# Kernel tuning notes

Hardware: AMD Instinct MI355X
Metric: run time of the kernel (lower is better)

Reference implementation:

```python
import jax, jax.numpy as jnp
import numpy as np

B, N, DIM = 8, 1024, 1024
H, DH = 16, 64           # heads, dim_head; inner_dim = H*DH = 1024
SCALE = DH ** -0.5


def setup_inputs() -> dict:
    key = jax.random.key(0)
    k_x, k_qkv, k_out, k_b = jax.random.split(key, 4)
    inner = H * DH
    x = jax.random.normal(k_x, (B, N, DIM), dtype=jnp.float32)
    # nn.Linear(dim, inner*3, bias=False): y = x @ W_qkv
    W_qkv = jax.random.normal(k_qkv, (DIM, 3 * inner), dtype=jnp.float32) * (DIM ** -0.5)
    # nn.Linear(inner, dim) with bias (project_out is True since heads!=1)
    W_out = jax.random.normal(k_out, (inner, DIM), dtype=jnp.float32) * (inner ** -0.5)
    b_out = jax.random.normal(k_b, (DIM,), dtype=jnp.float32) * 0.01
    return {"x": x, "W_qkv": W_qkv, "W_out": W_out, "b_out": b_out}


def reference(x, W_qkv, W_out, b_out):
    # 'trans' branch of Attention.forward (dropout p=0 -> identity)
    qkv = x @ W_qkv                                   # [b, n, 3*inner]
    q, k, v = jnp.split(qkv, 3, axis=-1)              # each [b, n, inner]
    def to_heads(t):
        b, n, _ = t.shape
        return t.reshape(b, n, H, DH).transpose(0, 2, 1, 3)  # [b, h, n, d]
    q, k, v = to_heads(q), to_heads(k), to_heads(v)
    dots = jnp.einsum('bhid,bhjd->bhij', q, k) * SCALE  # [b, h, n, n]
    attn = jax.nn.softmax(dots, axis=-1)
    out = jnp.einsum('bhij,bhjd->bhid', attn, v)        # [b, h, n, d]
    # original sets attn = out (b h n d) before merging heads
    attn_ret = out
    out_m = out.transpose(0, 2, 1, 3).reshape(B, N, H * DH)  # [b, n, inner]
    proj = out_m @ W_out + b_out                        # [b, n, dim]
    return (proj, attn_ret)
```

## Files before the change

kernel.cpp:

```cpp
#include <hip/hip_runtime.h>
#include <hip/hip_bf16.h>
#include <math.h>

typedef __bf16 bf16_t;
typedef __bf16 bf16x8 __attribute__((ext_vector_type(8)));
typedef __bf16 bf16x4 __attribute__((ext_vector_type(4)));
typedef float f32x4 __attribute__((ext_vector_type(4)));

#define MFMA16(a, b, c) __builtin_amdgcn_mfma_f32_16x16x32_bf16((a), (b), (c), 0, 0, 0)

#define AS3(p) ((__attribute__((address_space(3))) void*)(p))
#define AS1(p) ((const __attribute__((address_space(1))) void*)(p))

#define B_ 8
#define N_ 1024
#define DIM_ 1024
#define H_ 16
#define DH_ 64

#define QSCALE 0.18033688011112042f
#define SM_SHIFT 12.0f

__global__ __launch_bounds__(256) void k_prep(const float* __restrict__ x,
                                              bf16_t* __restrict__ xb,
                                              const float* __restrict__ Wqkv,
                                              bf16_t* __restrict__ wqkvt,
                                              const float* __restrict__ Wout,
                                              bf16_t* __restrict__ woutt) {
    int bx = blockIdx.x;
    int tid = threadIdx.x;
    if (bx < 4096) {
        size_t idx = ((size_t)bx * 256 + tid) * 8;
        f32x4 a = *(const f32x4*)(x + idx);
        f32x4 b = *(const f32x4*)(x + idx + 4);
        bf16x8 o;
        o[0] = (bf16_t)a[0]; o[1] = (bf16_t)a[1]; o[2] = (bf16_t)a[2]; o[3] = (bf16_t)a[3];
        o[4] = (bf16_t)b[0]; o[5] = (bf16_t)b[1]; o[6] = (bf16_t)b[2]; o[7] = (bf16_t)b[3];
        *(bf16x8*)(xb + idx) = o;
        return;
    }
    __shared__ float tile[32][33];
    int idx = bx - 4096;
    int rb = idx >> 7, cbx = idx & 127;
    const float* in;
    bf16_t* out;
    int C, cb;
    if (cbx < 96) { in = Wqkv; out = wqkvt; C = 3072; cb = cbx; }
    else          { in = Wout; out = woutt; C = 1024; cb = cbx - 96; }
    const int R = 1024;
    int c0 = cb * 32, r0 = rb * 32;
    int tx = tid & 31, ty = tid >> 5;
#pragma unroll
    for (int i = 0; i < 4; ++i)
        tile[ty + 8 * i][tx] = in[(size_t)(r0 + ty + 8 * i) * C + (c0 + tx)];
    __syncthreads();
#pragma unroll
    for (int i = 0; i < 4; ++i)
        out[(size_t)(c0 + ty + 8 * i) * R + (r0 + tx)] = (bf16_t)tile[tx][ty + 8 * i];
}

__global__ __launch_bounds__(512, 1) void k_gemm_qkv(const bf16_t* __restrict__ A,
                                                     const bf16_t* __restrict__ Bt,
                                                     bf16_t* __restrict__ qb,
                                                     bf16_t* __restrict__ kbuf,
                                                     bf16_t* __restrict__ vbuf) {
    __shared__ __align__(16) bf16_t As[2][256 * 64];
    __shared__ __align__(16) bf16_t Bs[2][256 * 64];
    int tid = threadIdx.x;
    int lane = tid & 63, wave = tid >> 6;
    int quad = lane >> 4, l16 = lane & 15;
    int wr = wave >> 2, wc = wave & 3;

    int bid = blockIdx.x;
    int swz = (bid & 7) * 48 + (bid >> 3);
    int mt = swz / 12, nt = swz % 12;
    int m0 = mt * 256, c0 = nt * 256;

    const f32x4 vzero = {0.f, 0.f, 0.f, 0.f};
    f32x4 acc[8][4];
#pragma unroll
    for (int i = 0; i < 8; ++i)
#pragma unroll
        for (int j = 0; j < 4; ++j) acc[i][j] = vzero;

    int s0 = ((quad) ^ (l16 & 7)) * 8;
    int s1 = ((4 + quad) ^ (l16 & 7)) * 8;

    auto stageA = [&](int t, int i) {
        int k0 = t * 64;
        bf16_t* Ad = &As[t & 1][0];
        int cid = tid + 512 * i;
        int row = cid >> 3;
        int g = (cid & 7) ^ (row & 7);
        __builtin_amdgcn_global_load_lds(
            AS1(A + (size_t)(m0 + row) * 1024 + k0 + g * 8), AS3(Ad + cid * 8), 16, 0, 0);
    };
    auto stageB = [&](int t, int i) {
        int k0 = t * 64;
        bf16_t* Bd = &Bs[t & 1][0];
        int cid = tid + 512 * i;
        int row = cid >> 3;
        int g = (cid & 7) ^ (row & 7);
        __builtin_amdgcn_global_load_lds(
            AS1(Bt + (size_t)(c0 + row) * 1024 + k0 + g * 8), AS3(Bd + cid * 8), 16, 0, 0);
    };
    auto stage_all = [&](int t) {
#pragma unroll
        for (int i = 0; i < 4; ++i) stageA(t, i);
#pragma unroll
        for (int i = 0; i < 4; ++i) stageB(t, i);
    };

    stage_all(0);
    stage_all(1);

#pragma unroll 2
    for (int t = 0; t < 16; ++t) {
        int cur = t & 1;
        if (t < 15)
            asm volatile("s_waitcnt vmcnt(8)" ::: "memory");
        else
            asm volatile("s_waitcnt vmcnt(0)" ::: "memory");
        __builtin_amdgcn_s_barrier();
        asm volatile("" ::: "memory");

        const bf16_t* Arow = &As[cur][0] + (size_t)(wr * 128 + l16) * 64;
        const bf16_t* Brow = &Bs[cur][0] + (size_t)(wc * 64 + l16) * 64;
        bool pre = (t + 2 < 16);

        bf16x8 af[4][2], bq0[2][2], bq1[2][2];

#pragma unroll
        for (int i = 0; i < 4; ++i) {
            af[i][0] = *(const bf16x8*)(Arow + (16 * i) * 64 + s0);
            af[i][1] = *(const bf16x8*)(Arow + (16 * i) * 64 + s1);
        }
#pragma unroll
        for (int j = 0; j < 2; ++j) {
            bq0[j][0] = *(const bf16x8*)(Brow + (16 * j) * 64 + s0);
            bq0[j][1] = *(const bf16x8*)(Brow + (16 * j) * 64 + s1);
        }
        asm volatile("" ::: "memory");
        __builtin_amdgcn_s_barrier();
        asm volatile("s_waitcnt lgkmcnt(0)" ::: "memory");
        __builtin_amdgcn_sched_barrier(0);
        __builtin_amdgcn_s_setprio(1);
#pragma unroll
        for (int i = 0; i < 4; ++i)
#pragma unroll
            for (int j = 0; j < 2; ++j) {
                acc[i][j] = MFMA16(af[i][0], bq0[j][0], acc[i][j]);
                acc[i][j] = MFMA16(af[i][1], bq0[j][1], acc[i][j]);
            }
        __builtin_amdgcn_s_setprio(0);
        asm volatile("" ::: "memory");
        __builtin_amdgcn_s_barrier();

#pragma unroll
        for (int j = 0; j < 2; ++j) {
            bq1[j][0] = *(const bf16x8*)(Brow + (32 + 16 * j) * 64 + s0);
            bq1[j][1] = *(const bf16x8*)(Brow + (32 + 16 * j) * 64 + s1);
        }
        if (pre) { stageA(t + 2, 0); stageA(t + 2, 2); }
        asm volatile("" ::: "memory");
        __builtin_amdgcn_s_barrier();
        asm volatile("s_waitcnt lgkmcnt(0)" ::: "memory");
        __builtin_amdgcn_sched_barrier(0);
        __builtin_amdgcn_s_setprio(1);
#pragma unroll
        for (int i = 0; i < 4; ++i)
#pragma unroll
            for (int j = 0; j < 2; ++j) {
                acc[i][2 + j] = MFMA16(af[i][0], bq1[j][0], acc[i][2 + j]);
                acc[i][2 + j] = MFMA16(af[i][1], bq1[j][1], acc[i][2 + j]);
            }
        __builtin_amdgcn_s_setprio(0);
        asm volatile("" ::: "memory");
        __builtin_amdgcn_s_barrier();

#pragma unroll
        for (int i = 0; i < 4; ++i) {
            af[i][0] = *(const bf16x8*)(Arow + (64 + 16 * i) * 64 + s0);
            af[i][1] = *(const bf16x8*)(Arow + (64 + 16 * i) * 64 + s1);
        }
        if (pre) {
#pragma unroll
            for (int i = 0; i < 4; ++i) stageB(t + 2, i);
        }
        asm volatile("" ::: "memory");
        __builtin_amdgcn_s_barrier();
        asm volatile("s_waitcnt lgkmcnt(0)" ::: "memory");
        __builtin_amdgcn_sched_barrier(0);
        __builtin_amdgcn_s_setprio(1);
#pragma unroll
        for (int i = 0; i < 4; ++i)
#pragma unroll
            for (int j = 0; j < 2; ++j) {
                acc[4 + i][2 + j] = MFMA16(af[i][0], bq1[j][0], acc[4 + i][2 + j]);
                acc[4 + i][2 + j] = MFMA16(af[i][1], bq1[j][1], acc[4 + i][2 + j]);
            }
        __builtin_amdgcn_s_setprio(0);
        asm volatile("" ::: "memory");
        __builtin_amdgcn_s_barrier();

        if (pre) { stageA(t + 2, 1); stageA(t + 2, 3); }
        asm volatile("" ::: "memory");
        __builtin_amdgcn_s_barrier();
        __builtin_amdgcn_sched_barrier(0);
        __builtin_amdgcn_s_setprio(1);
#pragma unroll
        for (int i = 0; i < 4; ++i)
#pragma unroll
            for (int j = 0; j < 2; ++j) {
                acc[4 + i][j] = MFMA16(af[i][0], bq0[j][0], acc[4 + i][j]);
                acc[4 + i][j] = MFMA16(af[i][1], bq0[j][1], acc[4 + i][j]);
            }
        __builtin_amdgcn_s_setprio(0);
        asm volatile("" ::: "memory");
        __builtin_amdgcn_s_barrier();
    }

    int tsel = nt >> 2;
    bf16_t* obase = (tsel == 0) ? qb : (tsel == 1) ? kbuf : vbuf;
    float scl = (tsel == 0) ? QSCALE : 1.0f;
#pragma unroll
    for (int i = 0; i < 8; ++i) {
#pragma unroll
        for (int r = 0; r < 4; ++r) {
            int m = m0 + wr * 128 + 16 * i + quad * 4 + r;
            int b = m >> 10, n = m & 1023;
#pragma unroll
            for (int j = 0; j < 4; ++j) {
                int cc = c0 + wc * 64 + 16 * j + l16;
                int ic = cc & 1023;
                int h = ic >> 6, d = ic & 63;
                obase[(((size_t)b * H_ + h) * N_ + n) * DH_ + d] = (bf16_t)(acc[i][j][r] * scl);
            }
        }
    }
}

__global__ __launch_bounds__(256) void k_prep_v(const bf16_t* __restrict__ in,
                                                bf16_t* __restrict__ out) {
    __shared__ bf16_t t[64][65];
    int bh = blockIdx.y;
    int n0 = blockIdx.x * 64;
    int tid = threadIdx.x;
    int r = tid >> 2, c = (tid & 3) * 16;
    const bf16_t* ip = in + ((size_t)bh * N_ + n0 + r) * DH_ + c;
    bf16x8 a = *(const bf16x8*)ip;
    bf16x8 b2 = *(const bf16x8*)(ip + 8);
#pragma unroll
    for (int e = 0; e < 8; ++e) { t[r][c + e] = a[e]; t[r][c + 8 + e] = b2[e]; }
    __syncthreads();
    bf16x8 o1, o2;
#pragma unroll
    for (int e = 0; e < 8; ++e) { o1[e] = t[c + e][r]; o2[e] = t[c + 8 + e][r]; }
    bf16_t* op = out + ((size_t)bh * DH_ + r) * N_ + n0 + c;
    *(bf16x8*)op = o1;
    *(bf16x8*)(op + 8) = o2;
}

__global__ __launch_bounds__(256, 2) void k_attn(const bf16_t* __restrict__ q,
                                                 const bf16_t* __restrict__ k,
                                                 const bf16_t* __restrict__ vt,
                                                 float* __restrict__ oattn,
                                                 bf16_t* __restrict__ outm) {
    __shared__ __align__(16) bf16_t Ks[64 * 64];
    __shared__ __align__(16) bf16_t Vs[64 * 64];
    __shared__ __align__(16) bf16_t Ps[4 * 4 * 16 * 72];
    int tid = threadIdx.x;
    int lane = tid & 63, wave = tid >> 6;
    int quad = lane >> 4, l16 = lane & 15;
    int qt = blockIdx.x & 3;
    int bh = blockIdx.x >> 2;
    int b = bh >> 4, h = bh & 15;

    const bf16_t* qp = q + ((size_t)bh * N_ + qt * 256 + wave * 64) * DH_;
    bf16x8 qa[4][2];
#pragma unroll
    for (int g = 0; g < 4; ++g)
#pragma unroll
        for (int c = 0; c < 2; ++c)
            qa[g][c] = *(const bf16x8*)(qp + (size_t)(g * 16 + l16) * DH_ + c * 32 + quad * 8);

    const bf16_t* kp = k + (size_t)bh * N_ * DH_;
    const bf16_t* vp = vt + (size_t)bh * DH_ * N_;
    bf16_t* Pw = Ps + wave * (4 * 16 * 72);

    const f32x4 vzero = {0.f, 0.f, 0.f, 0.f};
    f32x4 o[4][4];
#pragma unroll
    for (int g = 0; g < 4; ++g)
#pragma unroll
        for (int t = 0; t < 4; ++t) o[g][t] = vzero;
    float lsum[4] = {0.f, 0.f, 0.f, 0.f};

    for (int kb = 0; kb < 16; ++kb) {
#pragma unroll
        for (int i = 0; i < 2; ++i) {
            int cid = tid + 256 * i;
            int row = cid >> 3;
            int g = (cid & 7) ^ (row & 7);
            __builtin_amdgcn_global_load_lds(
                AS1(kp + (size_t)(kb * 64 + row) * DH_ + g * 8), AS3(Ks + cid * 8), 16, 0, 0);
            __builtin_amdgcn_global_load_lds(
                AS1(vp + (size_t)row * N_ + kb * 64 + g * 8), AS3(Vs + cid * 8), 16, 0, 0);
        }
        __syncthreads();

        f32x4 st[4][4];
#pragma unroll
        for (int jt = 0; jt < 4; ++jt) {
#pragma unroll
            for (int g = 0; g < 4; ++g) st[g][jt] = vzero;
#pragma unroll
            for (int c = 0; c < 2; ++c) {
                int s = (4 * c + quad) ^ (l16 & 7);
                bf16x8 kf = *(const bf16x8*)(Ks + (16 * jt + l16) * 64 + s * 8);
#pragma unroll
                for (int g = 0; g < 4; ++g)
                    st[g][jt] = MFMA16(kf, qa[g][c], st[g][jt]);
            }
        }

#pragma unroll
        for (int g = 0; g < 4; ++g) {
            float ps = 0.f;
#pragma unroll
            for (int jt = 0; jt < 4; ++jt) {
                bf16x4 pk;
#pragma unroll
                for (int r = 0; r < 4; ++r) {
                    float p = __builtin_amdgcn_exp2f(st[g][jt][r] - SM_SHIFT);
                    ps += p;
                    pk[r] = (bf16_t)p;
                }
                *(bf16x4*)(Pw + g * (16 * 72) + l16 * 72 + jt * 16 + quad * 4) = pk;
            }
            lsum[g] += ps;
        }

        bf16x8 pf[4][2];
#pragma unroll
        for (int g = 0; g < 4; ++g)
#pragma unroll
            for (int c = 0; c < 2; ++c)
                pf[g][c] = *(const bf16x8*)(Pw + g * (16 * 72) + l16 * 72 + c * 32 + quad * 8);
#pragma unroll
        for (int t = 0; t < 4; ++t)
#pragma unroll
            for (int c = 0; c < 2; ++c) {
                int s = (4 * c + quad) ^ (l16 & 7);
                bf16x8 vf = *(const bf16x8*)(Vs + (16 * t + l16) * 64 + s * 8);
#pragma unroll
                for (int g = 0; g < 4; ++g)
                    o[g][t] = MFMA16(vf, pf[g][c], o[g][t]);
            }
        __syncthreads();
    }

#pragma unroll
    for (int g = 0; g < 4; ++g) {
        lsum[g] += __shfl_xor(lsum[g], 16);
        lsum[g] += __shfl_xor(lsum[g], 32);
    }

    float* Ot = (float*)Ps + wave * 16 * 68;
#pragma unroll
    for (int g = 0; g < 4; ++g) {
        float inv = 1.f / lsum[g];
#pragma unroll
        for (int t = 0; t < 4; ++t) {
            f32x4 v4;
#pragma unroll
            for (int r = 0; r < 4; ++r) v4[r] = o[g][t][r] * inv;
            *(f32x4*)(Ot + l16 * 68 + t * 16 + quad * 4) = v4;
        }
        int row = lane >> 2, cl = lane & 3;
        int n = qt * 256 + wave * 64 + g * 16 + row;
        const float* orow = Ot + row * 68 + cl * 16;
        float* gout = oattn + ((size_t)bh * N_ + n) * DH_ + cl * 16;
        bf16_t* gm = outm + ((size_t)b * N_ + n) * DIM_ + h * DH_ + cl * 16;
#pragma unroll
        for (int s = 0; s < 4; ++s) {
            f32x4 v = *(const f32x4*)(orow + s * 4);
            *(f32x4*)(gout + s * 4) = v;
            bf16x4 vb;
#pragma unroll
            for (int r = 0; r < 4; ++r) vb[r] = (bf16_t)v[r];
            *(bf16x4*)(gm + s * 4) = vb;
        }
    }
}

__global__ __launch_bounds__(256) void k_gemm_proj(const bf16_t* __restrict__ A,
                                                   const bf16_t* __restrict__ Bt,
                                                   const float* __restrict__ bias,
                                                   float* __restrict__ out) {
    __shared__ __align__(16) bf16_t As[128 * 64];
    __shared__ __align__(16) bf16_t Bs[128 * 64];
    int tid = threadIdx.x;
    int lane = tid & 63, wave = tid >> 6;
    int quad = lane >> 4, l16 = lane & 15;
    int m0 = blockIdx.y * 128, c0 = blockIdx.x * 128;
    int wm = (wave & 1) * 64, wn = (wave >> 1) * 64;

    const f32x4 vzero = {0.f, 0.f, 0.f, 0.f};
    f32x4 acc[4][4];
#pragma unroll
    for (int i = 0; i < 4; ++i)
#pragma unroll
        for (int j = 0; j < 4; ++j) acc[i][j] = vzero;

    for (int k0 = 0; k0 < 1024; k0 += 64) {
#pragma unroll
        for (int i = 0; i < 4; ++i) {
            int cid = tid + 256 * i;
            int row = cid >> 3;
            int g = (cid & 7) ^ (row & 7);
            __builtin_amdgcn_global_load_lds(
                AS1(A + (size_t)(m0 + row) * 1024 + k0 + g * 8), AS3(As + cid * 8), 16, 0, 0);
            __builtin_amdgcn_global_load_lds(
                AS1(Bt + (size_t)(c0 + row) * 1024 + k0 + g * 8), AS3(Bs + cid * 8), 16, 0, 0);
        }
        __syncthreads();
#pragma unroll
        for (int c = 0; c < 2; ++c) {
            int s = (4 * c + quad) ^ (l16 & 7);
            bf16x8 bfr[4];
#pragma unroll
            for (int j = 0; j < 4; ++j)
                bfr[j] = *(const bf16x8*)(Bs + (wn + 16 * j + l16) * 64 + s * 8);
#pragma unroll
            for (int i = 0; i < 4; ++i) {
                bf16x8 af = *(const bf16x8*)(As + (wm + 16 * i + l16) * 64 + s * 8);
#pragma unroll
                for (int j = 0; j < 4; ++j)
                    acc[i][j] = MFMA16(af, bfr[j], acc[i][j]);
            }
        }
        __syncthreads();
    }

#pragma unroll
    for (int i = 0; i < 4; ++i) {
#pragma unroll
        for (int r = 0; r < 4; ++r) {
            int m = m0 + wm + 16 * i + quad * 4 + r;
#pragma unroll
            for (int j = 0; j < 4; ++j) {
                int cc = c0 + wn + 16 * j + l16;
                out[(size_t)m * DIM_ + cc] = acc[i][j][r] + bias[cc];
            }
        }
    }
}

extern "C" void kernel_launch(void* const* d_in, const int* in_sizes, int n_in,
                              void* d_out, int out_size, void* d_ws, size_t ws_size,
                              hipStream_t stream) {
    const float* x    = (const float*)d_in[0];
    const float* Wqkv = (const float*)d_in[1];
    const float* Wout = (const float*)d_in[2];
    const float* bout = (const float*)d_in[3];

    float* proj  = (float*)d_out;
    float* oattn = proj + (size_t)B_ * N_ * DIM_;

    char* ws = (char*)d_ws;
    const size_t MB = 1024 * 1024;
    bf16_t* xb    = (bf16_t*)(ws);
    bf16_t* wqkvt = (bf16_t*)(ws + 16 * MB);
    bf16_t* woutt = (bf16_t*)(ws + 22 * MB);
    bf16_t* qb    = (bf16_t*)(ws + 24 * MB);
    bf16_t* kbuf  = (bf16_t*)(ws + 40 * MB);
    bf16_t* vtb   = (bf16_t*)(ws + 56 * MB);
    bf16_t* outm  = (bf16_t*)(ws + 72 * MB);
    bf16_t* vbuf  = outm;

    k_prep<<<8192, 256, 0, stream>>>(x, xb, Wqkv, wqkvt, Wout, woutt);
    k_gemm_qkv<<<384, 512, 0, stream>>>(xb, wqkvt, qb, kbuf, vbuf);
    k_prep_v<<<dim3(16, 128), 256, 0, stream>>>(vbuf, vtb);
    k_attn<<<512, 256, 0, stream>>>(qb, kbuf, vtb, oattn, outm);
    k_gemm_proj<<<dim3(8, 64), 256, 0, stream>>>(outm, woutt, bout, proj);
}
```

Measured before the change: 253.5 us.

## Retile QKV GEMM to 256x192, double-buffer attention KV and projection GEMM

```diff
diff --git a/kernel.cpp b/kernel.cpp
--- a/kernel.cpp
+++ b/kernel.cpp
@@ -65,23 +65,23 @@
                                                      bf16_t* __restrict__ kbuf,
                                                      bf16_t* __restrict__ vbuf) {
     __shared__ __align__(16) bf16_t As[2][256 * 64];
-    __shared__ __align__(16) bf16_t Bs[2][256 * 64];
+    __shared__ __align__(16) bf16_t Bs[2][192 * 64];
     int tid = threadIdx.x;
     int lane = tid & 63, wave = tid >> 6;
     int quad = lane >> 4, l16 = lane & 15;
     int wr = wave >> 2, wc = wave & 3;
 
     int bid = blockIdx.x;
-    int swz = (bid & 7) * 48 + (bid >> 3);
-    int mt = swz / 12, nt = swz % 12;
-    int m0 = mt * 256, c0 = nt * 256;
+    int swz = (bid & 7) * 64 + (bid >> 3);
+    int mt = swz >> 4, nt = swz & 15;
+    int m0 = mt * 256, c0 = nt * 192;
 
     const f32x4 vzero = {0.f, 0.f, 0.f, 0.f};
-    f32x4 acc[8][4];
+    f32x4 acc[8][3];
 #pragma unroll
     for (int i = 0; i < 8; ++i)
 #pragma unroll
-        for (int j = 0; j < 4; ++j) acc[i][j] = vzero;
+        for (int j = 0; j < 3; ++j) acc[i][j] = vzero;
 
     int s0 = ((quad) ^ (l16 & 7)) * 8;
     int s1 = ((4 + quad) ^ (l16 & 7)) * 8;
@@ -108,7 +108,7 @@
 #pragma unroll
         for (int i = 0; i < 4; ++i) stageA(t, i);
 #pragma unroll
-        for (int i = 0; i < 4; ++i) stageB(t, i);
+        for (int i = 0; i < 3; ++i) stageB(t, i);
     };
 
     stage_all(0);
@@ -118,17 +118,17 @@
     for (int t = 0; t < 16; ++t) {
         int cur = t & 1;
         if (t < 15)
-            asm volatile("s_waitcnt vmcnt(8)" ::: "memory");
+            asm volatile("s_waitcnt vmcnt(7)" ::: "memory");
         else
             asm volatile("s_waitcnt vmcnt(0)" ::: "memory");
         __builtin_amdgcn_s_barrier();
         asm volatile("" ::: "memory");
 
         const bf16_t* Arow = &As[cur][0] + (size_t)(wr * 128 + l16) * 64;
-        const bf16_t* Brow = &Bs[cur][0] + (size_t)(wc * 64 + l16) * 64;
+        const bf16_t* Brow = &Bs[cur][0] + (size_t)(wc * 48 + l16) * 64;
         bool pre = (t + 2 < 16);
 
-        bf16x8 af[4][2], bq0[2][2], bq1[2][2];
+        bf16x8 af[4][2], bq[2][2], b2[2];
 
 #pragma unroll
         for (int i = 0; i < 4; ++i) {
@@ -137,8 +137,8 @@
         }
 #pragma unroll
         for (int j = 0; j < 2; ++j) {
-            bq0[j][0] = *(const bf16x8*)(Brow + (16 * j) * 64 + s0);
-            bq0[j][1] = *(const bf16x8*)(Brow + (16 * j) * 64 + s1);
+            bq[j][0] = *(const bf16x8*)(Brow + (16 * j) * 64 + s0);
+            bq[j][1] = *(const bf16x8*)(Brow + (16 * j) * 64 + s1);
         }
         asm volatile("" ::: "memory");
         __builtin_amdgcn_s_barrier();
@@ -149,18 +149,15 @@
         for (int i = 0; i < 4; ++i)
 #pragma unroll
             for (int j = 0; j < 2; ++j) {
-                acc[i][j] = MFMA16(af[i][0], bq0[j][0], acc[i][j]);
-                acc[i][j] = MFMA16(af[i][1], bq0[j][1], acc[i][j]);
+                acc[i][j] = MFMA16(af[i][0], bq[j][0], acc[i][j]);
+                acc[i][j] = MFMA16(af[i][1], bq[j][1], acc[i][j]);
             }
         __builtin_amdgcn_s_setprio(0);
         asm volatile("" ::: "memory");
         __builtin_amdgcn_s_barrier();
 
-#pragma unroll
-        for (int j = 0; j < 2; ++j) {
-            bq1[j][0] = *(const bf16x8*)(Brow + (32 + 16 * j) * 64 + s0);
-            bq1[j][1] = *(const bf16x8*)(Brow + (32 + 16 * j) * 64 + s1);
-        }
+        b2[0] = *(const bf16x8*)(Brow + 32 * 64 + s0);
+        b2[1] = *(const bf16x8*)(Brow + 32 * 64 + s1);
         if (pre) { stageA(t + 2, 0); stageA(t + 2, 2); }
         asm volatile("" ::: "memory");
         __builtin_amdgcn_s_barrier();
@@ -168,12 +165,10 @@
         __builtin_amdgcn_sched_barrier(0);
         __builtin_amdgcn_s_setprio(1);
 #pragma unroll
-        for (int i = 0; i < 4; ++i)
-#pragma unroll
-            for (int j = 0; j < 2; ++j) {
-                acc[i][2 + j] = MFMA16(af[i][0], bq1[j][0], acc[i][2 + j]);
-                acc[i][2 + j] = MFMA16(af[i][1], bq1[j][1], acc[i][2 + j]);
-            }
+        for (int i = 0; i < 4; ++i) {
+            acc[i][2] = MFMA16(af[i][0], b2[0], acc[i][2]);
+            acc[i][2] = MFMA16(af[i][1], b2[1], acc[i][2]);
+        }
         __builtin_amdgcn_s_setprio(0);
         asm volatile("" ::: "memory");
         __builtin_amdgcn_s_barrier();
@@ -185,7 +180,7 @@
         }
         if (pre) {
 #pragma unroll
-            for (int i = 0; i < 4; ++i) stageB(t + 2, i);
+            for (int i = 0; i < 3; ++i) stageB(t + 2, i);
         }
         asm volatile("" ::: "memory");
         __builtin_amdgcn_s_barrier();
@@ -193,12 +188,10 @@
         __builtin_amdgcn_sched_barrier(0);
         __builtin_amdgcn_s_setprio(1);
 #pragma unroll
-        for (int i = 0; i < 4; ++i)
-#pragma unroll
-            for (int j = 0; j < 2; ++j) {
-                acc[4 + i][2 + j] = MFMA16(af[i][0], bq1[j][0], acc[4 + i][2 + j]);
-                acc[4 + i][2 + j] = MFMA16(af[i][1], bq1[j][1], acc[4 + i][2 + j]);
-            }
+        for (int i = 0; i < 4; ++i) {
+            acc[4 + i][2] = MFMA16(af[i][0], b2[0], acc[4 + i][2]);
+            acc[4 + i][2] = MFMA16(af[i][1], b2[1], acc[4 + i][2]);
+        }
         __builtin_amdgcn_s_setprio(0);
         asm volatile("" ::: "memory");
         __builtin_amdgcn_s_barrier();
@@ -212,17 +205,14 @@
         for (int i = 0; i < 4; ++i)
 #pragma unroll
             for (int j = 0; j < 2; ++j) {
-                acc[4 + i][j] = MFMA16(af[i][0], bq0[j][0], acc[4 + i][j]);
-                acc[4 + i][j] = MFMA16(af[i][1], bq0[j][1], acc[4 + i][j]);
+                acc[4 + i][j] = MFMA16(af[i][0], bq[j][0], acc[4 + i][j]);
+                acc[4 + i][j] = MFMA16(af[i][1], bq[j][1], acc[4 + i][j]);
             }
         __builtin_amdgcn_s_setprio(0);
         asm volatile("" ::: "memory");
         __builtin_amdgcn_s_barrier();
     }
 
-    int tsel = nt >> 2;
-    bf16_t* obase = (tsel == 0) ? qb : (tsel == 1) ? kbuf : vbuf;
-    float scl = (tsel == 0) ? QSCALE : 1.0f;
 #pragma unroll
     for (int i = 0; i < 8; ++i) {
 #pragma unroll
@@ -230,10 +220,13 @@
             int m = m0 + wr * 128 + 16 * i + quad * 4 + r;
             int b = m >> 10, n = m & 1023;
 #pragma unroll
-            for (int j = 0; j < 4; ++j) {
-                int cc = c0 + wc * 64 + 16 * j + l16;
+            for (int j = 0; j < 3; ++j) {
+                int cc = c0 + wc * 48 + 16 * j + l16;
+                int tsel = cc >> 10;
                 int ic = cc & 1023;
                 int h = ic >> 6, d = ic & 63;
+                bf16_t* obase = (tsel == 0) ? qb : (tsel == 1) ? kbuf : vbuf;
+                float scl = (tsel == 0) ? QSCALE : 1.0f;
                 obase[(((size_t)b * H_ + h) * N_ + n) * DH_ + d] = (bf16_t)(acc[i][j][r] * scl);
             }
         }
@@ -266,8 +259,8 @@
                                                  const bf16_t* __restrict__ vt,
                                                  float* __restrict__ oattn,
                                                  bf16_t* __restrict__ outm) {
-    __shared__ __align__(16) bf16_t Ks[64 * 64];
-    __shared__ __align__(16) bf16_t Vs[64 * 64];
+    __shared__ __align__(16) bf16_t Ks[2][64 * 64];
+    __shared__ __align__(16) bf16_t Vs[2][64 * 64];
     __shared__ __align__(16) bf16_t Ps[4 * 4 * 16 * 72];
     int tid = threadIdx.x;
     int lane = tid & 63, wave = tid >> 6;
@@ -288,26 +281,43 @@
     const bf16_t* vp = vt + (size_t)bh * DH_ * N_;
     bf16_t* Pw = Ps + wave * (4 * 16 * 72);
 
-    const f32x4 vzero = {0.f, 0.f, 0.f, 0.f};
-    f32x4 o[4][4];
-#pragma unroll
-    for (int g = 0; g < 4; ++g)
-#pragma unroll
-        for (int t = 0; t < 4; ++t) o[g][t] = vzero;
-    float lsum[4] = {0.f, 0.f, 0.f, 0.f};
-
-    for (int kb = 0; kb < 16; ++kb) {
+    auto stageKV = [&](int kb) {
 #pragma unroll
         for (int i = 0; i < 2; ++i) {
             int cid = tid + 256 * i;
             int row = cid >> 3;
             int g = (cid & 7) ^ (row & 7);
             __builtin_amdgcn_global_load_lds(
-                AS1(kp + (size_t)(kb * 64 + row) * DH_ + g * 8), AS3(Ks + cid * 8), 16, 0, 0);
+                AS1(kp + (size_t)(kb * 64 + row) * DH_ + g * 8),
+                AS3(&Ks[kb & 1][0] + cid * 8), 16, 0, 0);
             __builtin_amdgcn_global_load_lds(
-                AS1(vp + (size_t)row * N_ + kb * 64 + g * 8), AS3(Vs + cid * 8), 16, 0, 0);
-        }
-        __syncthreads();
+                AS1(vp + (size_t)row * N_ + kb * 64 + g * 8),
+                AS3(&Vs[kb & 1][0] + cid * 8), 16, 0, 0);
+        }
+    };
+
+    const f32x4 vzero = {0.f, 0.f, 0.f, 0.f};
+    f32x4 o[4][4];
+#pragma unroll
+    for (int g = 0; g < 4; ++g)
+#pragma unroll
+        for (int t = 0; t < 4; ++t) o[g][t] = vzero;
+    float lsum[4] = {0.f, 0.f, 0.f, 0.f};
+
+    stageKV(0);
+    stageKV(1);
+
+    for (int kb = 0; kb < 16; ++kb) {
+        int cur = kb & 1;
+        if (kb < 15)
+            asm volatile("s_waitcnt vmcnt(4)" ::: "memory");
+        else
+            asm volatile("s_waitcnt vmcnt(0)" ::: "memory");
+        __builtin_amdgcn_s_barrier();
+        asm volatile("" ::: "memory");
+
+        const bf16_t* Kc = &Ks[cur][0];
+        const bf16_t* Vc = &Vs[cur][0];
 
         f32x4 st[4][4];
 #pragma unroll
@@ -317,7 +327,7 @@
 #pragma unroll
             for (int c = 0; c < 2; ++c) {
                 int s = (4 * c + quad) ^ (l16 & 7);
-                bf16x8 kf = *(const bf16x8*)(Ks + (16 * jt + l16) * 64 + s * 8);
+                bf16x8 kf = *(const bf16x8*)(Kc + (16 * jt + l16) * 64 + s * 8);
 #pragma unroll
                 for (int g = 0; g < 4; ++g)
                     st[g][jt] = MFMA16(kf, qa[g][c], st[g][jt]);
@@ -352,12 +362,16 @@
 #pragma unroll
             for (int c = 0; c < 2; ++c) {
                 int s = (4 * c + quad) ^ (l16 & 7);
-                bf16x8 vf = *(const bf16x8*)(Vs + (16 * t + l16) * 64 + s * 8);
+                bf16x8 vf = *(const bf16x8*)(Vc + (16 * t + l16) * 64 + s * 8);
 #pragma unroll
                 for (int g = 0; g < 4; ++g)
                     o[g][t] = MFMA16(vf, pf[g][c], o[g][t]);
             }
-        __syncthreads();
+
+        asm volatile("" ::: "memory");
+        __builtin_amdgcn_s_barrier();
+        asm volatile("" ::: "memory");
+        if (kb + 2 < 16) stageKV(kb + 2);
     }
 
 #pragma unroll
@@ -394,17 +408,21 @@
     }
 }
 
-__global__ __launch_bounds__(256) void k_gemm_proj(const bf16_t* __restrict__ A,
-                                                   const bf16_t* __restrict__ Bt,
-                                                   const float* __restrict__ bias,
-                                                   float* __restrict__ out) {
-    __shared__ __align__(16) bf16_t As[128 * 64];
-    __shared__ __align__(16) bf16_t Bs[128 * 64];
+__global__ __launch_bounds__(256, 2) void k_gemm_proj(const bf16_t* __restrict__ A,
+                                                      const bf16_t* __restrict__ Bt,
+                                                      const float* __restrict__ bias,
+                                                      float* __restrict__ out) {
+    __shared__ __align__(16) bf16_t As[2][128 * 64];
+    __shared__ __align__(16) bf16_t Bs[2][128 * 64];
     int tid = threadIdx.x;
     int lane = tid & 63, wave = tid >> 6;
     int quad = lane >> 4, l16 = lane & 15;
-    int m0 = blockIdx.y * 128, c0 = blockIdx.x * 128;
     int wm = (wave & 1) * 64, wn = (wave >> 1) * 64;
+
+    int bid = blockIdx.x;
+    int swz = (bid & 7) * 64 + (bid >> 3);
+    int mt = swz >> 3, nt = swz & 7;
+    int m0 = mt * 128, c0 = nt * 128;
 
     const f32x4 vzero = {0.f, 0.f, 0.f, 0.f};
     f32x4 acc[4][4];
@@ -413,34 +431,107 @@
 #pragma unroll
         for (int j = 0; j < 4; ++j) acc[i][j] = vzero;
 
-    for (int k0 = 0; k0 < 1024; k0 += 64) {
+    int s0 = ((quad) ^ (l16 & 7)) * 8;
+    int s1 = ((4 + quad) ^ (l16 & 7)) * 8;
+
+    auto stageA = [&](int t, int i) {
+        int k0 = t * 64;
+        bf16_t* Ad = &As[t & 1][0];
+        int cid = tid + 256 * i;
+        int row = cid >> 3;
+        int g = (cid & 7) ^ (row & 7);
+        __builtin_amdgcn_global_load_lds(
+            AS1(A + (size_t)(m0 + row) * 1024 + k0 + g * 8), AS3(Ad + cid * 8), 16, 0, 0);
+    };
+    auto stageB = [&](int t, int i) {
+        int k0 = t * 64;
+        bf16_t* Bd = &Bs[t & 1][0];
+        int cid = tid + 256 * i;
+        int row = cid >> 3;
+        int g = (cid & 7) ^ (row & 7);
+        __builtin_amdgcn_global_load_lds(
+            AS1(Bt + (size_t)(c0 + row) * 1024 + k0 + g * 8), AS3(Bd + cid * 8), 16, 0, 0);
+    };
+    auto stage_all = [&](int t) {
+#pragma unroll
+        for (int i = 0; i < 4; ++i) stageA(t, i);
+#pragma unroll
+        for (int i = 0; i < 4; ++i) stageB(t, i);
+    };
+
+    stage_all(0);
+    stage_all(1);
+
+#pragma unroll 2
+    for (int t = 0; t < 16; ++t) {
+        int cur = t & 1;
+        if (t < 15)
+            asm volatile("s_waitcnt vmcnt(8)" ::: "memory");
+        else
+            asm volatile("s_waitcnt vmcnt(0)" ::: "memory");
+        __builtin_amdgcn_s_barrier();
+        asm volatile("" ::: "memory");
+
+        const bf16_t* Arow = &As[cur][0] + (size_t)(wm + l16) * 64;
+        const bf16_t* Brow = &Bs[cur][0] + (size_t)(wn + l16) * 64;
+        bool pre = (t + 2 < 16);
+
+        bf16x8 af[4][2], bq0[2][2], bq1[2][2];
+
 #pragma unroll
         for (int i = 0; i < 4; ++i) {
-            int cid = tid + 256 * i;
-            int row = cid >> 3;
-            int g = (cid & 7) ^ (row & 7);
-            __builtin_amdgcn_global_load_lds(
-                AS1(A + (size_t)(m0 + row) * 1024 + k0 + g * 8), AS3(As + cid * 8), 16, 0, 0);
-            __builtin_amdgcn_global_load_lds(
-                AS1(Bt + (size_t)(c0 + row) * 1024 + k0 + g * 8), AS3(Bs + cid * 8), 16, 0, 0);
-        }
-        __syncthreads();
-#pragma unroll
-        for (int c = 0; c < 2; ++c) {
-            int s = (4 * c + quad) ^ (l16 & 7);
-            bf16x8 bfr[4];
-#pragma unroll
-            for (int j = 0; j < 4; ++j)
-                bfr[j] = *(const bf16x8*)(Bs + (wn + 16 * j + l16) * 64 + s * 8);
-#pragma unroll
-            for (int i = 0; i < 4; ++i) {
-                bf16x8 af = *(const bf16x8*)(As + (wm + 16 * i + l16) * 64 + s * 8);
-#pragma unroll
-                for (int j = 0; j < 4; ++j)
-                    acc[i][j] = MFMA16(af, bfr[j], acc[i][j]);
-            }
-        }
-        __syncthreads();
+            af[i][0] = *(const bf16x8*)(Arow + (16 * i) * 64 + s0);
+            af[i][1] = *(const bf16x8*)(Arow + (16 * i) * 64 + s1);
+        }
+#pragma unroll
+        for (int j = 0; j < 2; ++j) {
+            bq0[j][0] = *(const bf16x8*)(Brow + (16 * j) * 64 + s0);
+            bq0[j][1] = *(const bf16x8*)(Brow + (16 * j) * 64 + s1);
+        }
+        asm volatile("" ::: "memory");
+        __builtin_amdgcn_s_barrier();
+        asm volatile("s_waitcnt lgkmcnt(0)" ::: "memory");
+        __builtin_amdgcn_sched_barrier(0);
+        __builtin_amdgcn_s_setprio(1);
+#pragma unroll
+        for (int i = 0; i < 4; ++i)
+#pragma unroll
+            for (int j = 0; j < 2; ++j) {
+                acc[i][j] = MFMA16(af[i][0], bq0[j][0], acc[i][j]);
+                acc[i][j] = MFMA16(af[i][1], bq0[j][1], acc[i][j]);
+            }
+        __builtin_amdgcn_s_setprio(0);
+        asm volatile("" ::: "memory");
+        __builtin_amdgcn_s_barrier();
+
+#pragma unroll
+        for (int j = 0; j < 2; ++j) {
+            bq1[j][0] = *(const bf16x8*)(Brow + (32 + 16 * j) * 64 + s0);
+            bq1[j][1] = *(const bf16x8*)(Brow + (32 + 16 * j) * 64 + s1);
+        }
+        if (pre) {
+#pragma unroll
+            for (int i = 0; i < 4; ++i) stageA(t + 2, i);
+        }
+        asm volatile("" ::: "memory");
+        __builtin_amdgcn_s_barrier();
+        asm volatile("s_waitcnt lgkmcnt(0)" ::: "memory");
+        __builtin_amdgcn_sched_barrier(0);
+        __builtin_amdgcn_s_setprio(1);
+#pragma unroll
+        for (int i = 0; i < 4; ++i)
+#pragma unroll
+            for (int j = 0; j < 2; ++j) {
+                acc[i][2 + j] = MFMA16(af[i][0], bq1[j][0], acc[i][2 + j]);
+                acc[i][2 + j] = MFMA16(af[i][1], bq1[j][1], acc[i][2 + j]);
+            }
+        __builtin_amdgcn_s_setprio(0);
+        asm volatile("" ::: "memory");
+        __builtin_amdgcn_s_barrier();
+        if (pre) {
+#pragma unroll
+            for (int i = 0; i < 4; ++i) stageB(t + 2, i);
+        }
     }
 
 #pragma unroll
@@ -480,8 +571,8 @@
     bf16_t* vbuf  = outm;
 
     k_prep<<<8192, 256, 0, stream>>>(x, xb, Wqkv, wqkvt, Wout, woutt);
-    k_gemm_qkv<<<384, 512, 0, stream>>>(xb, wqkvt, qb, kbuf, vbuf);
+    k_gemm_qkv<<<512, 512, 0, stream>>>(xb, wqkvt, qb, kbuf, vbuf);
     k_prep_v<<<dim3(16, 128), 256, 0, stream>>>(vbuf, vtb);
     k_attn<<<512, 256, 0, stream>>>(qb, kbuf, vtb, oattn, outm);
-    k_gemm_proj<<<dim3(8, 64), 256, 0, stream>>>(outm, woutt, bout, proj);
+    k_gemm_proj<<<512, 256, 0, stream>>>(outm, woutt, bout, proj);
 }
```

Result: faster. 239.3 us (-5.6%).
